# Kernel tuning notes

Hardware: AMD Instinct MI355X
Metric: run time of the kernel (lower is better)

Reference implementation:

```python
import jax, jax.numpy as jnp
import numpy as np

N_NODES = 100000
N_EDGES = 1600000
DIM = 128
N_BUNDLES = 8
BUNDLE_DIM = 4
HIDDEN = 256
TIME = 2


def setup_inputs() -> dict:
    key = jax.random.key(0)
    ks = jax.random.split(key, 8)
    x = jax.random.normal(ks[0], (N_NODES, DIM), dtype=jnp.float32)
    node_rep = jax.random.normal(ks[1], (N_NODES, N_BUNDLES, BUNDLE_DIM, BUNDLE_DIM), dtype=jnp.float32)
    # edge list; ensure every node has out-degree >= 1 so degree norm is finite
    src_extra = jax.random.randint(ks[2], (N_EDGES - N_NODES,), 0, N_NODES)
    src = jnp.concatenate([jnp.arange(N_NODES), src_extra]).astype(jnp.int64)
    dst = jax.random.randint(ks[3], (N_EDGES,), 0, N_NODES).astype(jnp.int64)
    w1 = jax.random.normal(ks[4], (HIDDEN, DIM), dtype=jnp.float32) * (1.0 / np.sqrt(DIM))
    b1 = jnp.zeros((HIDDEN,), dtype=jnp.float32)
    w2 = jax.random.normal(ks[5], (DIM, HIDDEN), dtype=jnp.float32) * (1.0 / np.sqrt(HIDDEN))
    b2 = jnp.zeros((DIM,), dtype=jnp.float32)
    return {"x": x, "node_rep": node_rep, "src": src, "dst": dst,
            "w1": w1, "b1": b1, "w2": w2, "b2": b2}


def reference(x, node_rep, src, dst, w1, b1, w2, b2):
    n = x.shape[0]
    # out-degrees (number of edges with node as source)
    deg = jax.ops.segment_sum(jnp.ones_like(src, dtype=x.dtype), src, num_segments=n)
    # u_mul_v: per-edge product of src and dst degrees -> symmetric norm coefs
    norm_coefs = jax.lax.rsqrt(deg[src] * deg[dst])  # [E]
    # per-bundle rotation: einsum('abcd,abde->abce', node_rep, vf)
    vf = x.reshape(n, N_BUNDLES, BUNDLE_DIM, -1)
    vf = jnp.einsum('nbcd,nbde->nbce', node_rep, vf)
    h = vf.reshape(n, DIM)
    # u_mul_e_sum repeated `time` times: out[dst] += h[src] * coef
    for _ in range(TIME):
        h = jax.ops.segment_sum(h[src] * norm_coefs[:, None], dst, num_segments=n)
    # inverse rotation with transposed node_rep
    vf = h.reshape(n, N_BUNDLES, BUNDLE_DIM, -1)
    vf = jnp.einsum('nbdc,nbde->nbce', node_rep, vf)
    h = vf.reshape(n, DIM)
    # feed-forward (dropout=0, exact GELU as in torch nn.GELU default)
    h = jax.nn.gelu(h @ w1.T + b1, approximate=False)
    return h @ w2.T + b2
```

## Files before the change

### kernel.cpp

```cpp
#include <hip/hip_runtime.h>
#include <hip/hip_bf16.h>
#include <math.h>

#define DIM 128
#define HID 256

typedef short s8x __attribute__((ext_vector_type(8)));
typedef float f4x __attribute__((ext_vector_type(4)));

__device__ __forceinline__ unsigned short f2bf(float f) {
    unsigned int u = __float_as_uint(f);
    u += 0x7FFF + ((u >> 16) & 1);
    return (unsigned short)(u >> 16);
}
__device__ __forceinline__ float bf2f(unsigned short b) {
    return __uint_as_float(((unsigned int)b) << 16);
}
__device__ __forceinline__ float bflo(unsigned int p) {
    return __uint_as_float(p << 16);
}
__device__ __forceinline__ float bfhi(unsigned int p) {
    return __uint_as_float(p & 0xffff0000u);
}


__global__ __launch_bounds__(256) void hist_kernel(
        const int* __restrict__ src, const int* __restrict__ dst,
        int* __restrict__ TD, int* __restrict__ TS, int nE, int nbuck, int chunk) {
    __shared__ int hd[1024], hs[1024];
    const int tid = threadIdx.x, blk = blockIdx.x;
    for (int b = tid; b < nbuck; b += 256) { hd[b] = 0; hs[b] = 0; }
    __syncthreads();
    int beg = blk * chunk, end = min(beg + chunk, nE);
    for (int i = beg + tid; i < end; i += 256) {
        atomicAdd(&hd[dst[i] >> 7], 1);
        atomicAdd(&hs[src[i] >> 7], 1);
    }
    __syncthreads();
    for (int b = tid; b < nbuck; b += 256) {
        TD[b * 256 + blk] = hd[b];
        TS[b * 256 + blk] = hs[b];
    }
}

__global__ void scan_blocks(const int* in, int* out, int* bsums, int n) {
    __shared__ int part[256];
    const int tid = threadIdx.x;
    const int base = blockIdx.x * 1024 + tid * 4;
    int v[4];
    int sum = 0;
#pragma unroll
    for (int k = 0; k < 4; ++k) {
        v[k] = (base + k < n) ? in[base + k] : 0;
        sum += v[k];
    }
    part[tid] = sum;
    __syncthreads();
    for (int off = 1; off < 256; off <<= 1) {
        int t = (tid >= off) ? part[tid - off] : 0;
        __syncthreads();
        part[tid] += t;
        __syncthreads();
    }
    int excl = part[tid] - sum;
    if (tid == 255) bsums[blockIdx.x] = part[255];
#pragma unroll
    for (int k = 0; k < 4; ++k) {
        if (base + k < n) out[base + k] = excl;
        excl += v[k];
    }
}

__global__ void scan_sums(int* bsums, int nb) {
    __shared__ int part[256];
    const int tid = threadIdx.x;
    const int base = tid * 4;
    int v[4];
    int sum = 0;
#pragma unroll
    for (int k = 0; k < 4; ++k) {
        v[k] = (base + k < nb) ? bsums[base + k] : 0;
        sum += v[k];
    }
    part[tid] = sum;
    __syncthreads();
    for (int off = 1; off < 256; off <<= 1) {
        int t = (tid >= off) ? part[tid - off] : 0;
        __syncthreads();
        part[tid] += t;
        __syncthreads();
    }
    int excl = part[tid] - sum;
#pragma unroll
    for (int k = 0; k < 4; ++k) {
        if (base + k < nb) bsums[base + k] = excl;
        excl += v[k];
    }
}

__global__ void scan_add(int* T, const int* __restrict__ bsums, int n2, int half, int E) {
    int i = blockIdx.x * blockDim.x + threadIdx.x;
    if (i < n2) {
        int v = T[i] + bsums[i >> 10];
        T[i] = (i >= half) ? v - E : v;
    }
}

__global__ __launch_bounds__(256) void scatter_edges(
        const int* __restrict__ src, const int* __restrict__ dst,
        const int* __restrict__ TD, const int* __restrict__ TS,
        unsigned int* __restrict__ pairs, unsigned char* __restrict__ sbyte,
        int nE, int nbuck, int chunk) {
    __shared__ int cd[1024], cs[1024];
    const int tid = threadIdx.x, blk = blockIdx.x;
    for (int b = tid; b < nbuck; b += 256) {
        cd[b] = TD[b * 256 + blk];
        cs[b] = TS[b * 256 + blk];
    }
    __syncthreads();
    int beg = blk * chunk, end = min(beg + chunk, nE);
    for (int i = beg + tid; i < end; i += 256) {
        int s = src[i], d = dst[i];
        int pd = atomicAdd(&cd[d >> 7], 1);
        pairs[pd] = ((unsigned)s << 7) | (unsigned)(d & 127);
        int ps = atomicAdd(&cs[s >> 7], 1);
        sbyte[ps] = (unsigned char)(s & 127);
    }
}

__global__ __launch_bounds__(256) void finalize_src(
        const unsigned char* __restrict__ sbyte, const int* __restrict__ TS,
        float* __restrict__ rdeg, int nE, int nbuck, int nN) {
    __shared__ int hist[128];
    const int tid = threadIdx.x, b = blockIdx.x;
    if (tid < 128) hist[tid] = 0;
    __syncthreads();
    int beg = TS[b * 256];
    int end = (b + 1 < nbuck) ? TS[(b + 1) * 256] : nE;
    for (int i = beg + tid; i < end; i += 256)
        atomicAdd(&hist[sbyte[i]], 1);
    __syncthreads();
    if (tid < 128) {
        int idx = (b << 7) + tid;
        if (idx < nN) rdeg[idx] = rsqrtf((float)hist[tid]);
    }
}

template<bool PACK>
__global__ __launch_bounds__(256) void finalize_dst(
        const unsigned int* __restrict__ pairs, const int* __restrict__ TD,
        const float* __restrict__ rdeg,
        int* __restrict__ rowstart, uint2* __restrict__ ecsr,
        int* __restrict__ esrcA, int nE, int nbuck, int nN) {
    __shared__ int hist[128], sbuf[128], cur[128];
    const int tid = threadIdx.x, b = blockIdx.x;
    int beg = TD[b * 256];
    int end = (b + 1 < nbuck) ? TD[(b + 1) * 256] : nE;
    if (tid < 128) hist[tid] = 0;
    __syncthreads();
    for (int i = beg + tid; i < end; i += 256)
        atomicAdd(&hist[(int)(pairs[i] & 127u)], 1);
    __syncthreads();
    int v = (tid < 128) ? hist[tid] : 0;
    if (tid < 128) sbuf[tid] = v;
    __syncthreads();
    for (int off = 1; off < 128; off <<= 1) {
        int t = (tid < 128 && tid >= off) ? sbuf[tid - off] : 0;
        __syncthreads();
        if (tid < 128) sbuf[tid] += t;
        __syncthreads();
    }
    if (tid < 128) {
        int excl = sbuf[tid] - v;
        cur[tid] = excl;
        int idx = (b << 7) + tid;
        if (idx <= nN) rowstart[idx] = beg + excl;
    }
    __syncthreads();
    for (int i = beg + tid; i < end; i += 256) {
        unsigned int p = pairs[i];
        int l = (int)(p & 127u);
        int s = (int)(p >> 7);
        int pos = atomicAdd(&cur[l], 1);
        if (PACK) {
            float coef = rdeg[s] * rdeg[(b << 7) + l];
            ecsr[beg + pos] = make_uint2((unsigned)s, __float_as_uint(coef));
        } else {
            esrcA[beg + pos] = s;
        }
    }
}

__global__ void rot_cvt_kernel(const float* __restrict__ x, const float* __restrict__ R,
                               unsigned short* __restrict__ h0,
                               const float* __restrict__ w1, const float* __restrict__ w2,
                               unsigned short* __restrict__ w1b, unsigned short* __restrict__ w2b,
                               int n, int nbRot) {
    if ((int)blockIdx.x >= nbRot) {
        int t = (blockIdx.x - nbRot) * 256 + threadIdx.x;
        for (int i = t; i < 32768; i += 4096) {
            w1b[i] = f2bf(w1[i]);
            w2b[i] = f2bf(w2[i]);
        }
        return;
    }
    int u = blockIdx.x * blockDim.x + threadIdx.x;
    if (u >= n * 8) return;
    int nd = u >> 3, b = u & 7;
    const float* xp = &x[(size_t)nd * DIM + b * 16];
    const float* Rp = &R[(size_t)nd * DIM + b * 16];
    float xv[16], rv[16];
#pragma unroll
    for (int d = 0; d < 4; ++d) {
        *(float4*)&xv[d * 4] = *(const float4*)&xp[d * 4];
        *(float4*)&rv[d * 4] = *(const float4*)&Rp[d * 4];
    }
    unsigned short ob[16];
#pragma unroll
    for (int c = 0; c < 4; ++c)
#pragma unroll
        for (int e = 0; e < 4; ++e) {
            float acc = 0.f;
#pragma unroll
            for (int d = 0; d < 4; ++d) acc += rv[c * 4 + d] * xv[d * 4 + e];
            ob[c * 4 + e] = f2bf(acc);
        }
    unsigned short* op = &h0[(size_t)nd * DIM + b * 16];
    *(s8x*)&op[0] = *(s8x*)&ob[0];
    *(s8x*)&op[8] = *(s8x*)&ob[8];
}

template<bool PACK>
__global__ __launch_bounds__(256) void gather_kernel(
        const unsigned short* __restrict__ hsrc,
        const uint2* __restrict__ ecsr, const int* __restrict__ esrcA,
        const float* __restrict__ rdeg, const int* __restrict__ rowstart,
        unsigned short* __restrict__ hdst, int n) {
    const int node = blockIdx.x * 16 + (threadIdx.x >> 4);
    const int lane = threadIdx.x & 15;
    if (node >= n) return;
    const int beg = rowstart[node];
    const int end = rowstart[node + 1];
    float rd = 0.f;
    if (!PACK) rd = rdeg[node];
    float a0 = 0.f, a1 = 0.f, a2 = 0.f, a3 = 0.f;
    float a4 = 0.f, a5 = 0.f, a6 = 0.f, a7 = 0.f;
    int i = beg;
    for (; i + 2 <= end; i += 2) {
        int s0, s1;
        float c0, c1;
        if (PACK) {
            uint2 e0 = ecsr[i], e1 = ecsr[i + 1];
            s0 = (int)e0.x; c0 = __uint_as_float(e0.y);
            s1 = (int)e1.x; c1 = __uint_as_float(e1.y);
        } else {
            s0 = esrcA[i]; s1 = esrcA[i + 1];
            c0 = rdeg[s0] * rd; c1 = rdeg[s1] * rd;
        }
        uint4 p0 = *(const uint4*)&hsrc[(size_t)s0 * DIM + lane * 8];
        uint4 p1 = *(const uint4*)&hsrc[(size_t)s1 * DIM + lane * 8];
        a0 += bflo(p0.x) * c0 + bflo(p1.x) * c1;
        a1 += bfhi(p0.x) * c0 + bfhi(p1.x) * c1;
        a2 += bflo(p0.y) * c0 + bflo(p1.y) * c1;
        a3 += bfhi(p0.y) * c0 + bfhi(p1.y) * c1;
        a4 += bflo(p0.z) * c0 + bflo(p1.z) * c1;
        a5 += bfhi(p0.z) * c0 + bfhi(p1.z) * c1;
        a6 += bflo(p0.w) * c0 + bflo(p1.w) * c1;
        a7 += bfhi(p0.w) * c0 + bfhi(p1.w) * c1;
    }
    if (i < end) {
        int s0;
        float c0;
        if (PACK) {
            uint2 e0 = ecsr[i];
            s0 = (int)e0.x; c0 = __uint_as_float(e0.y);
        } else {
            s0 = esrcA[i];
            c0 = rdeg[s0] * rd;
        }
        uint4 p0 = *(const uint4*)&hsrc[(size_t)s0 * DIM + lane * 8];
        a0 += bflo(p0.x) * c0;
        a1 += bfhi(p0.x) * c0;
        a2 += bflo(p0.y) * c0;
        a3 += bfhi(p0.y) * c0;
        a4 += bflo(p0.z) * c0;
        a5 += bfhi(p0.z) * c0;
        a6 += bflo(p0.w) * c0;
        a7 += bfhi(p0.w) * c0;
    }
    uint4 o;
    o.x = (unsigned)f2bf(a0) | ((unsigned)f2bf(a1) << 16);
    o.y = (unsigned)f2bf(a2) | ((unsigned)f2bf(a3) << 16);
    o.z = (unsigned)f2bf(a4) | ((unsigned)f2bf(a5) << 16);
    o.w = (unsigned)f2bf(a6) | ((unsigned)f2bf(a7) << 16);
    *(uint4*)&hdst[(size_t)node * DIM + lane * 8] = o;
}

#define ABST 136
#define HBST 264
__global__ __launch_bounds__(256, 4) void ffn_kernel(
        const unsigned short* __restrict__ h,
        const float* __restrict__ R,
        const unsigned short* __restrict__ w1b,
        const float* __restrict__ b1,
        const unsigned short* __restrict__ w2b,
        const float* __restrict__ b2,
        float* __restrict__ out, int n) {
    __shared__ unsigned short smem[64 * HBST];
    unsigned short* abuf = smem;
    unsigned short* hbuf = smem;
    const int tid  = threadIdx.x;
    const int node0 = blockIdx.x * 64;
    const int wave = tid >> 6;
    const int lane = tid & 63;
    const int lr = lane & 15;
    const int lq = lane >> 4;

    for (int u = tid; u < 512; u += 256) {
        int nd = u >> 3, b = u & 7;
        int gn = node0 + nd;
        float hv[16], rv[16];
        if (gn < n) {
            const unsigned short* hp = &h[(size_t)gn * DIM + b * 16];
            const float* Rp = &R[(size_t)gn * DIM + b * 16];
            unsigned short hraw[16];
            *(s8x*)&hraw[0] = *(const s8x*)&hp[0];
            *(s8x*)&hraw[8] = *(const s8x*)&hp[8];
#pragma unroll
            for (int d = 0; d < 16; ++d) hv[d] = bf2f(hraw[d]);
#pragma unroll
            for (int d = 0; d < 4; ++d)
                *(float4*)&rv[d * 4] = *(const float4*)&Rp[d * 4];
        } else {
#pragma unroll
            for (int d = 0; d < 16; ++d) { hv[d] = 0.f; rv[d] = 0.f; }
        }
#pragma unroll
        for (int c = 0; c < 4; ++c) {
            unsigned short gb[4];
#pragma unroll
            for (int e = 0; e < 4; ++e) {
                float acc = 0.f;
#pragma unroll
                for (int d = 0; d < 4; ++d) acc += rv[d * 4 + c] * hv[d * 4 + e];
                gb[e] = f2bf(acc);
            }
            *(ushort4*)&abuf[nd * ABST + b * 16 + c * 4] =
                make_ushort4(gb[0], gb[1], gb[2], gb[3]);
        }
    }
    __syncthreads();

    f4x acc1[4][4];
#pragma unroll
    for (int mt = 0; mt < 4; ++mt)
#pragma unroll
        for (int nt = 0; nt < 4; ++nt) acc1[mt][nt] = (f4x){0.f, 0.f, 0.f, 0.f};

    const int nw = wave * 64;
    for (int ks = 0; ks < 4; ++ks) {
        const int k0 = ks * 32 + lq * 8;
        s8x af[4], bfv[4];
#pragma unroll
        for (int mt = 0; mt < 4; ++mt)
            af[mt] = *(const s8x*)&abuf[(mt * 16 + lr) * ABST + k0];
#pragma unroll
        for (int nt = 0; nt < 4; ++nt)
            bfv[nt] = *(const s8x*)&w1b[(size_t)(nw + nt * 16 + lr) * 128 + k0];
#pragma unroll
        for (int mt = 0; mt < 4; ++mt)
#pragma unroll
            for (int nt = 0; nt < 4; ++nt)
                acc1[mt][nt] = __builtin_amdgcn_mfma_f32_16x16x32_bf16(
                    af[mt], bfv[nt], acc1[mt][nt], 0, 0, 0);
    }
    __syncthreads();

#pragma unroll
    for (int nt = 0; nt < 4; ++nt) {
        int nn = nw + nt * 16 + lr;
        float bias = b1[nn];
#pragma unroll
        for (int mt = 0; mt < 4; ++mt) {
#pragma unroll
            for (int r = 0; r < 4; ++r) {
                float v = acc1[mt][nt][r] + bias;
                v = 0.5f * v * (1.f + erff(v * 0.70710678118654752f));
                hbuf[(mt * 16 + lq * 4 + r) * HBST + nn] = f2bf(v);
            }
        }
    }
    __syncthreads();

    f4x acc2[4][2];
#pragma unroll
    for (int mt = 0; mt < 4; ++mt)
#pragma unroll
        for (int nt = 0; nt < 2; ++nt) acc2[mt][nt] = (f4x){0.f, 0.f, 0.f, 0.f};

    const int nw2 = wave * 32;
    for (int ks = 0; ks < 8; ++ks) {
        const int k0 = ks * 32 + lq * 8;
        s8x af[4], bf2v[2];
#pragma unroll
        for (int mt = 0; mt < 4; ++mt)
            af[mt] = *(const s8x*)&hbuf[(mt * 16 + lr) * HBST + k0];
#pragma unroll
        for (int nt = 0; nt < 2; ++nt)
            bf2v[nt] = *(const s8x*)&w2b[(size_t)(nw2 + nt * 16 + lr) * 256 + k0];
#pragma unroll
        for (int mt = 0; mt < 4; ++mt)
#pragma unroll
            for (int nt = 0; nt < 2; ++nt)
                acc2[mt][nt] = __builtin_amdgcn_mfma_f32_16x16x32_bf16(
                    af[mt], bf2v[nt], acc2[mt][nt], 0, 0, 0);
    }
#pragma unroll
    for (int nt = 0; nt < 2; ++nt) {
        int n2 = nw2 + nt * 16 + lr;
        float bias = b2[n2];
#pragma unroll
        for (int mt = 0; mt < 4; ++mt) {
#pragma unroll
            for (int r = 0; r < 4; ++r) {
                int gn = node0 + mt * 16 + lq * 4 + r;
                if (gn < n) out[(size_t)gn * DIM + n2] = acc2[mt][nt][r] + bias;
            }
        }
    }
}

extern "C" void kernel_launch(void* const* d_in, const int* in_sizes, int n_in,
                              void* d_out, int out_size, void* d_ws, size_t ws_size,
                              hipStream_t stream) {
    const float* x   = (const float*)d_in[0];
    const float* R   = (const float*)d_in[1];
    const int*   src = (const int*)d_in[2];
    const int*   dst = (const int*)d_in[3];
    const float* w1  = (const float*)d_in[4];
    const float* b1  = (const float*)d_in[5];
    const float* w2  = (const float*)d_in[6];
    const float* b2  = (const float*)d_in[7];
    float* out = (float*)d_out;

    const int N = in_sizes[0] / DIM;
    const int E = in_sizes[2];

    const int nbuck = (N + 127) >> 7;
    const int chunk = (E + 255) / 256;
    const int nScan = nbuck * 256;
    const int nScan2 = 2 * nScan;
    const int nbScan2 = (nScan2 + 1023) / 1024;

    unsigned short* hA = (unsigned short*)d_ws;
    unsigned short* hM = hA + (size_t)N * DIM;
    unsigned int*  pairs = (unsigned int*)hM;
    unsigned char* sbyte = (unsigned char*)(pairs + E);
    char* edge_base = (char*)(hM + (size_t)N * DIM);

    const size_t tail_bytes = (size_t)N * 4 + (size_t)(N + 1) * 4 +
                              (size_t)nScan * 8 + 1024 * 4 + 2 * 32768 * 2;
    const size_t fixed_bytes = (size_t)N * DIM * 4;
    const bool use_pack = (fixed_bytes + (size_t)E * 8 + tail_bytes) <= ws_size;
    const size_t edge_bytes = use_pack ? (size_t)E * 8 : (size_t)E * 4;

    uint2* ecsr  = (uint2*)edge_base;
    int*   esrcA = (int*)edge_base;
    char* q = edge_base + edge_bytes;
    float* rdeg     = (float*)q;
    int*   rowstart = (int*)(rdeg + N);
    int*   TD       = rowstart + (N + 1);
    int*   TS       = TD + nScan;
    int*   bsums    = TS + nScan;
    unsigned short* w1b = (unsigned short*)(bsums + 1024);
    unsigned short* w2b = w1b + 32768;

    const int BLK = 256;

    hist_kernel<<<256, BLK, 0, stream>>>(src, dst, TD, TS, E, nbuck, chunk);
    scan_blocks<<<nbScan2, BLK, 0, stream>>>(TD, TD, bsums, nScan2);
    scan_sums<<<1, BLK, 0, stream>>>(bsums, nbScan2);
    scan_add<<<(nScan2 + BLK - 1) / BLK, BLK, 0, stream>>>(TD, bsums, nScan2, nScan, E);
    scatter_edges<<<256, BLK, 0, stream>>>(src, dst, TD, TS, pairs, sbyte, E, nbuck, chunk);
    finalize_src<<<nbuck, BLK, 0, stream>>>(sbyte, TS, rdeg, E, nbuck, N);
    if (use_pack)
        finalize_dst<true><<<nbuck, BLK, 0, stream>>>(pairs, TD, rdeg, rowstart,
                                                      ecsr, esrcA, E, nbuck, N);
    else
        finalize_dst<false><<<nbuck, BLK, 0, stream>>>(pairs, TD, rdeg, rowstart,
                                                       ecsr, esrcA, E, nbuck, N);

    const int nbRot = ((size_t)N * 8 + BLK - 1) / BLK;
    rot_cvt_kernel<<<nbRot + 16, BLK, 0, stream>>>(x, R, hA, w1, w2, w1b, w2b, N, nbRot);

    const int nbG = (N + 15) / 16;
    if (use_pack) {
        gather_kernel<true><<<nbG, BLK, 0, stream>>>(hA, ecsr, esrcA, rdeg,
                                                     rowstart, hM, N);
        gather_kernel<true><<<nbG, BLK, 0, stream>>>(hM, ecsr, esrcA, rdeg,
                                                     rowstart, hA, N);
    } else {
        gather_kernel<false><<<nbG, BLK, 0, stream>>>(hA, ecsr, esrcA, rdeg,
                                                      rowstart, hM, N);
        gather_kernel<false><<<nbG, BLK, 0, stream>>>(hM, ecsr, esrcA, rdeg,
                                                      rowstart, hA, N);
    }

    ffn_kernel<<<(N + 63) / 64, BLK, 0, stream>>>(hA, R, w1b, b1, w2b, b2, out, N);
}
```

Measured before the change: 430.7 us.

## Use more blocks for edge bucketing, unroll gather by four, shrink FFN tile

The histogram and scatter stages now run on up to 1024 blocks instead of 256, which spreads edge partitioning across more CUs. The scan-sum kernel is widened to handle the larger partial table, and the workspace layout is adjusted to fit it. The gather loop processes four edges per iteration, giving more loads in flight. The FFN kernel uses 32-node tiles with less shared memory and a higher occupancy hint. In exchange, scan work grows and each FFN block reuses its weight fragments less.

```diff
diff --git a/kernel.cpp b/kernel.cpp
--- a/kernel.cpp
+++ b/kernel.cpp
@@ -26,7 +26,8 @@
 
 __global__ __launch_bounds__(256) void hist_kernel(
         const int* __restrict__ src, const int* __restrict__ dst,
-        int* __restrict__ TD, int* __restrict__ TS, int nE, int nbuck, int chunk) {
+        int* __restrict__ TD, int* __restrict__ TS, int nE, int nbuck, int chunk,
+        int NBE) {
     __shared__ int hd[1024], hs[1024];
     const int tid = threadIdx.x, blk = blockIdx.x;
     for (int b = tid; b < nbuck; b += 256) { hd[b] = 0; hs[b] = 0; }
@@ -38,8 +39,8 @@
     }
     __syncthreads();
     for (int b = tid; b < nbuck; b += 256) {
-        TD[b * 256 + blk] = hd[b];
-        TS[b * 256 + blk] = hs[b];
+        TD[b * NBE + blk] = hd[b];
+        TS[b * NBE + blk] = hs[b];
     }
 }
 
@@ -74,11 +75,11 @@
 __global__ void scan_sums(int* bsums, int nb) {
     __shared__ int part[256];
     const int tid = threadIdx.x;
-    const int base = tid * 4;
-    int v[4];
+    const int base = tid * 8;
+    int v[8];
     int sum = 0;
 #pragma unroll
-    for (int k = 0; k < 4; ++k) {
+    for (int k = 0; k < 8; ++k) {
         v[k] = (base + k < nb) ? bsums[base + k] : 0;
         sum += v[k];
     }
@@ -92,7 +93,7 @@
     }
     int excl = part[tid] - sum;
 #pragma unroll
-    for (int k = 0; k < 4; ++k) {
+    for (int k = 0; k < 8; ++k) {
         if (base + k < nb) bsums[base + k] = excl;
         excl += v[k];
     }
@@ -110,12 +111,12 @@
         const int* __restrict__ src, const int* __restrict__ dst,
         const int* __restrict__ TD, const int* __restrict__ TS,
         unsigned int* __restrict__ pairs, unsigned char* __restrict__ sbyte,
-        int nE, int nbuck, int chunk) {
+        int nE, int nbuck, int chunk, int NBE) {
     __shared__ int cd[1024], cs[1024];
     const int tid = threadIdx.x, blk = blockIdx.x;
     for (int b = tid; b < nbuck; b += 256) {
-        cd[b] = TD[b * 256 + blk];
-        cs[b] = TS[b * 256 + blk];
+        cd[b] = TD[b * NBE + blk];
+        cs[b] = TS[b * NBE + blk];
     }
     __syncthreads();
     int beg = blk * chunk, end = min(beg + chunk, nE);
@@ -130,13 +131,13 @@
 
 __global__ __launch_bounds__(256) void finalize_src(
         const unsigned char* __restrict__ sbyte, const int* __restrict__ TS,
-        float* __restrict__ rdeg, int nE, int nbuck, int nN) {
+        float* __restrict__ rdeg, int nE, int nbuck, int nN, int NBE) {
     __shared__ int hist[128];
     const int tid = threadIdx.x, b = blockIdx.x;
     if (tid < 128) hist[tid] = 0;
     __syncthreads();
-    int beg = TS[b * 256];
-    int end = (b + 1 < nbuck) ? TS[(b + 1) * 256] : nE;
+    int beg = TS[b * NBE];
+    int end = (b + 1 < nbuck) ? TS[(b + 1) * NBE] : nE;
     for (int i = beg + tid; i < end; i += 256)
         atomicAdd(&hist[sbyte[i]], 1);
     __syncthreads();
@@ -151,11 +152,11 @@
         const unsigned int* __restrict__ pairs, const int* __restrict__ TD,
         const float* __restrict__ rdeg,
         int* __restrict__ rowstart, uint2* __restrict__ ecsr,
-        int* __restrict__ esrcA, int nE, int nbuck, int nN) {
+        int* __restrict__ esrcA, int nE, int nbuck, int nN, int NBE) {
     __shared__ int hist[128], sbuf[128], cur[128];
     const int tid = threadIdx.x, b = blockIdx.x;
-    int beg = TD[b * 256];
-    int end = (b + 1 < nbuck) ? TD[(b + 1) * 256] : nE;
+    int beg = TD[b * NBE];
+    int end = (b + 1 < nbuck) ? TD[(b + 1) * NBE] : nE;
     if (tid < 128) hist[tid] = 0;
     __syncthreads();
     for (int i = beg + tid; i < end; i += 256)
@@ -246,29 +247,34 @@
     float a0 = 0.f, a1 = 0.f, a2 = 0.f, a3 = 0.f;
     float a4 = 0.f, a5 = 0.f, a6 = 0.f, a7 = 0.f;
     int i = beg;
-    for (; i + 2 <= end; i += 2) {
-        int s0, s1;
-        float c0, c1;
+    for (; i + 4 <= end; i += 4) {
+        int s0, s1, s2, s3;
+        float c0, c1, c2, c3;
         if (PACK) {
-            uint2 e0 = ecsr[i], e1 = ecsr[i + 1];
+            uint2 e0 = ecsr[i], e1 = ecsr[i + 1], e2 = ecsr[i + 2], e3 = ecsr[i + 3];
             s0 = (int)e0.x; c0 = __uint_as_float(e0.y);
             s1 = (int)e1.x; c1 = __uint_as_float(e1.y);
+            s2 = (int)e2.x; c2 = __uint_as_float(e2.y);
+            s3 = (int)e3.x; c3 = __uint_as_float(e3.y);
         } else {
-            s0 = esrcA[i]; s1 = esrcA[i + 1];
+            s0 = esrcA[i]; s1 = esrcA[i + 1]; s2 = esrcA[i + 2]; s3 = esrcA[i + 3];
             c0 = rdeg[s0] * rd; c1 = rdeg[s1] * rd;
+            c2 = rdeg[s2] * rd; c3 = rdeg[s3] * rd;
         }
         uint4 p0 = *(const uint4*)&hsrc[(size_t)s0 * DIM + lane * 8];
         uint4 p1 = *(const uint4*)&hsrc[(size_t)s1 * DIM + lane * 8];
-        a0 += bflo(p0.x) * c0 + bflo(p1.x) * c1;
-        a1 += bfhi(p0.x) * c0 + bfhi(p1.x) * c1;
-        a2 += bflo(p0.y) * c0 + bflo(p1.y) * c1;
-        a3 += bfhi(p0.y) * c0 + bfhi(p1.y) * c1;
-        a4 += bflo(p0.z) * c0 + bflo(p1.z) * c1;
-        a5 += bfhi(p0.z) * c0 + bfhi(p1.z) * c1;
-        a6 += bflo(p0.w) * c0 + bflo(p1.w) * c1;
-        a7 += bfhi(p0.w) * c0 + bfhi(p1.w) * c1;
-    }
-    if (i < end) {
+        uint4 p2 = *(const uint4*)&hsrc[(size_t)s2 * DIM + lane * 8];
+        uint4 p3 = *(const uint4*)&hsrc[(size_t)s3 * DIM + lane * 8];
+        a0 += bflo(p0.x) * c0 + bflo(p1.x) * c1 + bflo(p2.x) * c2 + bflo(p3.x) * c3;
+        a1 += bfhi(p0.x) * c0 + bfhi(p1.x) * c1 + bfhi(p2.x) * c2 + bfhi(p3.x) * c3;
+        a2 += bflo(p0.y) * c0 + bflo(p1.y) * c1 + bflo(p2.y) * c2 + bflo(p3.y) * c3;
+        a3 += bfhi(p0.y) * c0 + bfhi(p1.y) * c1 + bfhi(p2.y) * c2 + bfhi(p3.y) * c3;
+        a4 += bflo(p0.z) * c0 + bflo(p1.z) * c1 + bflo(p2.z) * c2 + bflo(p3.z) * c3;
+        a5 += bfhi(p0.z) * c0 + bfhi(p1.z) * c1 + bfhi(p2.z) * c2 + bfhi(p3.z) * c3;
+        a6 += bflo(p0.w) * c0 + bflo(p1.w) * c1 + bflo(p2.w) * c2 + bflo(p3.w) * c3;
+        a7 += bfhi(p0.w) * c0 + bfhi(p1.w) * c1 + bfhi(p2.w) * c2 + bfhi(p3.w) * c3;
+    }
+    for (; i < end; ++i) {
         int s0;
         float c0;
         if (PACK) {
@@ -298,7 +304,7 @@
 
 #define ABST 136
 #define HBST 264
-__global__ __launch_bounds__(256, 4) void ffn_kernel(
+__global__ __launch_bounds__(256, 6) void ffn_kernel(
         const unsigned short* __restrict__ h,
         const float* __restrict__ R,
         const unsigned short* __restrict__ w1b,
@@ -306,18 +312,18 @@
         const unsigned short* __restrict__ w2b,
         const float* __restrict__ b2,
         float* __restrict__ out, int n) {
-    __shared__ unsigned short smem[64 * HBST];
+    __shared__ unsigned short smem[32 * HBST];
     unsigned short* abuf = smem;
     unsigned short* hbuf = smem;
     const int tid  = threadIdx.x;
-    const int node0 = blockIdx.x * 64;
+    const int node0 = blockIdx.x * 32;
     const int wave = tid >> 6;
     const int lane = tid & 63;
     const int lr = lane & 15;
     const int lq = lane >> 4;
 
-    for (int u = tid; u < 512; u += 256) {
-        int nd = u >> 3, b = u & 7;
+    {
+        int nd = tid >> 3, b = tid & 7;
         int gn = node0 + nd;
         float hv[16], rv[16];
         if (gn < n) {
@@ -351,24 +357,24 @@
     }
     __syncthreads();
 
-    f4x acc1[4][4];
-#pragma unroll
-    for (int mt = 0; mt < 4; ++mt)
+    f4x acc1[2][4];
+#pragma unroll
+    for (int mt = 0; mt < 2; ++mt)
 #pragma unroll
         for (int nt = 0; nt < 4; ++nt) acc1[mt][nt] = (f4x){0.f, 0.f, 0.f, 0.f};
 
     const int nw = wave * 64;
     for (int ks = 0; ks < 4; ++ks) {
         const int k0 = ks * 32 + lq * 8;
-        s8x af[4], bfv[4];
-#pragma unroll
-        for (int mt = 0; mt < 4; ++mt)
+        s8x af[2], bfv[4];
+#pragma unroll
+        for (int mt = 0; mt < 2; ++mt)
             af[mt] = *(const s8x*)&abuf[(mt * 16 + lr) * ABST + k0];
 #pragma unroll
         for (int nt = 0; nt < 4; ++nt)
             bfv[nt] = *(const s8x*)&w1b[(size_t)(nw + nt * 16 + lr) * 128 + k0];
 #pragma unroll
-        for (int mt = 0; mt < 4; ++mt)
+        for (int mt = 0; mt < 2; ++mt)
 #pragma unroll
             for (int nt = 0; nt < 4; ++nt)
                 acc1[mt][nt] = __builtin_amdgcn_mfma_f32_16x16x32_bf16(
@@ -381,7 +387,7 @@
         int nn = nw + nt * 16 + lr;
         float bias = b1[nn];
 #pragma unroll
-        for (int mt = 0; mt < 4; ++mt) {
+        for (int mt = 0; mt < 2; ++mt) {
 #pragma unroll
             for (int r = 0; r < 4; ++r) {
                 float v = acc1[mt][nt][r] + bias;
@@ -392,24 +398,24 @@
     }
     __syncthreads();
 
-    f4x acc2[4][2];
-#pragma unroll
-    for (int mt = 0; mt < 4; ++mt)
+    f4x acc2[2][2];
+#pragma unroll
+    for (int mt = 0; mt < 2; ++mt)
 #pragma unroll
         for (int nt = 0; nt < 2; ++nt) acc2[mt][nt] = (f4x){0.f, 0.f, 0.f, 0.f};
 
     const int nw2 = wave * 32;
     for (int ks = 0; ks < 8; ++ks) {
         const int k0 = ks * 32 + lq * 8;
-        s8x af[4], bf2v[2];
-#pragma unroll
-        for (int mt = 0; mt < 4; ++mt)
+        s8x af[2], bf2v[2];
+#pragma unroll
+        for (int mt = 0; mt < 2; ++mt)
             af[mt] = *(const s8x*)&hbuf[(mt * 16 + lr) * HBST + k0];
 #pragma unroll
         for (int nt = 0; nt < 2; ++nt)
             bf2v[nt] = *(const s8x*)&w2b[(size_t)(nw2 + nt * 16 + lr) * 256 + k0];
 #pragma unroll
-        for (int mt = 0; mt < 4; ++mt)
+        for (int mt = 0; mt < 2; ++mt)
 #pragma unroll
             for (int nt = 0; nt < 2; ++nt)
                 acc2[mt][nt] = __builtin_amdgcn_mfma_f32_16x16x32_bf16(
@@ -420,7 +426,7 @@
         int n2 = nw2 + nt * 16 + lr;
         float bias = b2[n2];
 #pragma unroll
-        for (int mt = 0; mt < 4; ++mt) {
+        for (int mt = 0; mt < 2; ++mt) {
 #pragma unroll
             for (int r = 0; r < 4; ++r) {
                 int gn = node0 + mt * 16 + lq * 4 + r;
@@ -447,8 +453,24 @@
     const int E = in_sizes[2];
 
     const int nbuck = (N + 127) >> 7;
-    const int chunk = (E + 255) / 256;
-    const int nScan = nbuck * 256;
+
+    const size_t fixed_bytes = (size_t)N * DIM * 4;
+    auto tail_bytes = [&](int nbe) {
+        return (size_t)N * 4 + (size_t)(N + 1) * 4 +
+               (size_t)nbuck * nbe * 8 + 2048 * 4 + (size_t)2 * 32768 * 2;
+    };
+    int NBE = 1024;
+    bool use_pack = true;
+    if (fixed_bytes + (size_t)E * 8 + tail_bytes(1024) > ws_size) {
+        if (fixed_bytes + (size_t)E * 8 + tail_bytes(256) <= ws_size) {
+            NBE = 256;
+        } else {
+            NBE = 256;
+            use_pack = false;
+        }
+    }
+    const int chunk = (E + NBE - 1) / NBE;
+    const int nScan = nbuck * NBE;
     const int nScan2 = 2 * nScan;
     const int nbScan2 = (nScan2 + 1023) / 1024;
 
@@ -457,11 +479,6 @@
     unsigned int*  pairs = (unsigned int*)hM;
     unsigned char* sbyte = (unsigned char*)(pairs + E);
     char* edge_base = (char*)(hM + (size_t)N * DIM);
-
-    const size_t tail_bytes = (size_t)N * 4 + (size_t)(N + 1) * 4 +
-                              (size_t)nScan * 8 + 1024 * 4 + 2 * 32768 * 2;
-    const size_t fixed_bytes = (size_t)N * DIM * 4;
-    const bool use_pack = (fixed_bytes + (size_t)E * 8 + tail_bytes) <= ws_size;
     const size_t edge_bytes = use_pack ? (size_t)E * 8 : (size_t)E * 4;
 
     uint2* ecsr  = (uint2*)edge_base;
@@ -472,23 +489,23 @@
     int*   TD       = rowstart + (N + 1);
     int*   TS       = TD + nScan;
     int*   bsums    = TS + nScan;
-    unsigned short* w1b = (unsigned short*)(bsums + 1024);
+    unsigned short* w1b = (unsigned short*)(bsums + 2048);
     unsigned short* w2b = w1b + 32768;
 
     const int BLK = 256;
 
-    hist_kernel<<<256, BLK, 0, stream>>>(src, dst, TD, TS, E, nbuck, chunk);
+    hist_kernel<<<NBE, BLK, 0, stream>>>(src, dst, TD, TS, E, nbuck, chunk, NBE);
     scan_blocks<<<nbScan2, BLK, 0, stream>>>(TD, TD, bsums, nScan2);
     scan_sums<<<1, BLK, 0, stream>>>(bsums, nbScan2);
     scan_add<<<(nScan2 + BLK - 1) / BLK, BLK, 0, stream>>>(TD, bsums, nScan2, nScan, E);
-    scatter_edges<<<256, BLK, 0, stream>>>(src, dst, TD, TS, pairs, sbyte, E, nbuck, chunk);
-    finalize_src<<<nbuck, BLK, 0, stream>>>(sbyte, TS, rdeg, E, nbuck, N);
+    scatter_edges<<<NBE, BLK, 0, stream>>>(src, dst, TD, TS, pairs, sbyte, E, nbuck, chunk, NBE);
+    finalize_src<<<nbuck, BLK, 0, stream>>>(sbyte, TS, rdeg, E, nbuck, N, NBE);
     if (use_pack)
         finalize_dst<true><<<nbuck, BLK, 0, stream>>>(pairs, TD, rdeg, rowstart,
-                                                      ecsr, esrcA, E, nbuck, N);
+                                                      ecsr, esrcA, E, nbuck, N, NBE);
     else
         finalize_dst<false><<<nbuck, BLK, 0, stream>>>(pairs, TD, rdeg, rowstart,
-                                                       ecsr, esrcA, E, nbuck, N);
+                                                       ecsr, esrcA, E, nbuck, N, NBE);
 
     const int nbRot = ((size_t)N * 8 + BLK - 1) / BLK;
     rot_cvt_kernel<<<nbRot + 16, BLK, 0, stream>>>(x, R, hA, w1, w2, w1b, w2b, N, nbRot);
@@ -506,5 +523,5 @@
                                                       rowstart, hA, N);
     }
 
-    ffn_kernel<<<(N + 63) / 64, BLK, 0, stream>>>(hA, R, w1b, b1, w2b, b2, out, N);
-}
+    ffn_kernel<<<(N + 31) / 32, BLK, 0, stream>>>(hA, R, w1b, b1, w2b, b2, out, N);
+}
```

Result: slower. 444.1 us (+3.1%).
